# Kernel optimization log

Hardware: AMD Instinct MI355X
Metric: run time of the kernel (lower is better)

The kernel has to match this reference:

```python
import jax, jax.numpy as jnp
import numpy as np
from jax import lax

ANCHOR_AREAS = (128.0**2, 256.0**2, 512.0**2)
ASPECT_RATIOS = (0.5, 1.0, 2.0)
STRIDE = 32.0                      # resnet backbone: get_orig_stat maps fm -> input via x*32
PRE_NMS_TOP_N = 2000
POST_NMS_TOP_N = 100
NMS_IOU_T = 0.7
SCORE_T = 0.1
MIN_SCALE = 0.01
BBOX_XFORM_CLIP = float(np.log(1000.0 / 16.0))


def make_anchors(H, W):
    # anchors laid out in (H, W, A) order to match the offset permutation below
    sizes = []
    for area in ANCHOR_AREAS:
        for r in ASPECT_RATIOS:          # aspect_ratio = w / h
            sizes.append((np.sqrt(area * r), np.sqrt(area / r)))
    sizes = jnp.asarray(np.asarray(sizes, dtype=np.float32))  # [A, 2] (w, h)
    cy = (jnp.arange(H, dtype=jnp.float32) + 0.5) * STRIDE
    cx = (jnp.arange(W, dtype=jnp.float32) + 0.5) * STRIDE
    cyg, cxg = jnp.meshgrid(cy, cx, indexing='ij')             # [H, W]
    cxg = cxg[:, :, None]
    cyg = cyg[:, :, None]
    w = sizes[:, 0]
    h = sizes[:, 1]
    anchors = jnp.stack([cxg - w / 2, cyg - h / 2, cxg + w / 2, cyg + h / 2], axis=-1)
    return anchors.reshape(-1, 4)                              # [H*W*A, 4] xyxy


def decode_boxes(anchors, offsets):
    # anchors [N,4], offsets [B,N,4] (tx, ty, tw, th) -> boxes [B,N,4] xyxy
    wa = anchors[:, 2] - anchors[:, 0]
    ha = anchors[:, 3] - anchors[:, 1]
    cxa = anchors[:, 0] + 0.5 * wa
    cya = anchors[:, 1] + 0.5 * ha
    tx, ty = offsets[..., 0], offsets[..., 1]
    tw = jnp.minimum(offsets[..., 2], BBOX_XFORM_CLIP)
    th = jnp.minimum(offsets[..., 3], BBOX_XFORM_CLIP)
    px = tx * wa + cxa
    py = ty * ha + cya
    pw = jnp.exp(tw) * wa
    ph = jnp.exp(th) * ha
    return jnp.stack([px - pw / 2, py - ph / 2, px + pw / 2, py + ph / 2], axis=-1)


def box_iou(a, b):
    area_a = (a[:, 2] - a[:, 0]) * (a[:, 3] - a[:, 1])
    area_b = (b[:, 2] - b[:, 0]) * (b[:, 3] - b[:, 1])
    lt = jnp.maximum(a[:, None, :2], b[None, :, :2])
    rb = jnp.minimum(a[:, None, 2:], b[None, :, 2:])
    wh = jnp.clip(rb - lt, 0.0)
    inter = wh[..., 0] * wh[..., 1]
    return inter / (area_a[:, None] + area_b[None, :] - inter + 1e-9)


def nms_single(boxes, scores):
    # boxes [P,4] sorted by descending score; invalid entries carry score -1
    P = boxes.shape[0]
    iou = box_iou(boxes, boxes)
    idx = jnp.arange(P)

    def body(i, keep):
        sup = (iou[i] > NMS_IOU_T) & (idx > i)
        return jnp.where(keep[i], keep & (~sup), keep)

    keep = lax.stop_gradient(lax.fori_loop(0, P, body, scores > 0.0))
    kept_scores = jnp.where(keep, scores, -1.0)
    top_s, top_i = lax.top_k(kept_scores, POST_NMS_TOP_N)
    return boxes[top_i], top_s


def rpn_forward(features, W1, b1, W2, b2, W3, b3):
    B, Cin, H, W = features.shape
    A = W3.shape[0]
    # 3x3 sliding conv + ReLU
    t = lax.conv_general_dilated(
        features, W1, window_strides=(1, 1), padding='SAME',
        dimension_numbers=('NCHW', 'OIHW', 'NCHW'))
    t = jax.nn.relu(t + b1[None, :, None, None])
    # 1x1 sibling heads as channel contractions
    offs = jnp.einsum('bchw,oc->bohw', t, W2) + b2[None, :, None, None]   # [B, A*4, H, W]
    logits = jnp.einsum('bchw,oc->bohw', t, W3) + b3[None, :, None, None]  # [B, A, H, W]
    # reorder to per-anchor layout (H, W, A)
    offs = offs.reshape(B, A, 4, H, W).transpose(0, 3, 4, 1, 2).reshape(B, -1, 4)
    scores = jax.nn.sigmoid(logits.transpose(0, 2, 3, 1).reshape(B, -1))  # [B, N]
    anchors = make_anchors(H, W)
    boxes = decode_boxes(anchors, offs)                                    # [B, N, 4]
    # clip to image boundary (handle_cross_boundary_boxes during testing)
    img_w, img_h = W * STRIDE, H * STRIDE
    boxes = jnp.stack([
        jnp.clip(boxes[..., 0], 0.0, img_w),
        jnp.clip(boxes[..., 1], 0.0, img_h),
        jnp.clip(boxes[..., 2], 0.0, img_w),
        jnp.clip(boxes[..., 3], 0.0, img_h)], axis=-1)
    # score-threshold + min-scale filtering
    bw = boxes[..., 2] - boxes[..., 0]
    bh = boxes[..., 3] - boxes[..., 1]
    valid = (scores >= SCORE_T) & (bw > MIN_SCALE * img_w) & (bh > MIN_SCALE * img_h)
    masked = jnp.where(valid, scores, -1.0)
    # pre-NMS top-k, then per-image NMS + post-NMS top-n
    top_s, top_i = lax.top_k(masked, PRE_NMS_TOP_N)                        # [B, P]
    top_boxes = jnp.take_along_axis(boxes, top_i[..., None], axis=1)       # [B, P, 4]
    out_boxes, out_scores = jax.vmap(nms_single)(top_boxes, top_s)
    return out_boxes, out_scores                                           # [B,100,4], [B,100]


def setup_inputs() -> dict:
    key = jax.random.key(0)
    ks = jax.random.split(key, 4)
    B, Cin, H, W = 8, 1024, 50, 50
    A = 9
    C = 512
    return {
        'features': jax.random.normal(ks[0], (B, Cin, H, W), jnp.float32),
        'W1': jax.random.normal(ks[1], (C, Cin, 3, 3), jnp.float32) * 0.01,
        'b1': jnp.zeros((C,), jnp.float32),
        'W2': jax.random.normal(ks[2], (A * 4, C), jnp.float32) * 0.01,
        'b2': jnp.zeros((A * 4,), jnp.float32),
        'W3': jax.random.normal(ks[3], (A, C), jnp.float32) * 0.01,
        'b3': jnp.zeros((A,), jnp.float32),
    }


def reference(features, W1, b1, W2, b2, W3, b3):
    return rpn_forward(features, W1, b1, W2, b2, W3, b3)
```

## Files before the change

kernel.cpp:

```cpp
#include <hip/hip_runtime.h>
#include <cstdint>

#define NB 8
#define CIN 1024
#define HDIM 50
#define WDIM 50
#define COUT 512
#define NA 9
#define NANCH (HDIM*WDIM*NA)
#define PRE_N 2000
#define POST_N 100

typedef __attribute__((ext_vector_type(8))) short bf16x8;
typedef __attribute__((ext_vector_type(4))) float f32x4;
typedef __attribute__((ext_vector_type(16))) float f32x16;
typedef __attribute__((ext_vector_type(8))) unsigned short ushort8v;

constexpr size_t TPLANE    = 20578304;
constexpr size_t OFF_TPH   = 0;
constexpr size_t OFF_TPL   = OFF_TPH + TPLANE;
constexpr size_t OFF_BOXES = 41156608;
constexpr size_t OFF_MS    = OFF_BOXES + 2880000;
constexpr size_t OFF_KEYS  = OFF_MS + 720000;
constexpr size_t OFF_TBOX  = OFF_KEYS + 1440000;
constexpr size_t OFF_TS    = OFF_TBOX + 256000;
constexpr size_t OFF_SUP   = OFF_TS + 64000;
constexpr size_t OFF_KEEP  = OFF_SUP + 4096000;
constexpr size_t PPLANE    = 44318720;
constexpr size_t OFF_PH    = 50614656;
constexpr size_t OFF_PL    = OFF_PH + PPLANE;
constexpr size_t WPLANE    = 9437184;
constexpr size_t OFF_WH    = OFF_PL + PPLANE;
constexpr size_t OFF_WL    = OFF_WH + WPLANE;

__device__ __forceinline__ void split2bf16(float v, unsigned short &hi, unsigned short &lo) {
    unsigned int u = __float_as_uint(v);
    unsigned int r = u + 0x7FFFu + ((u >> 16) & 1u);
    hi = (unsigned short)(r >> 16);
    float hf = __uint_as_float(((unsigned int)hi) << 16);
    float lf = v - hf;
    unsigned int u2 = __float_as_uint(lf);
    unsigned int r2 = u2 + 0x7FFFu + ((u2 >> 16) & 1u);
    lo = (unsigned short)(r2 >> 16);
}

__device__ __forceinline__ void gl_lds(const unsigned short* g, unsigned short* l) {
    __builtin_amdgcn_global_load_lds(
        (const __attribute__((address_space(1))) unsigned int*)(const void*)g,
        (__attribute__((address_space(3))) unsigned int*)(void*)l,
        16, 0, 0);
}

__global__ __launch_bounds__(256) void prep_feat(const float* __restrict__ f,
                                                 unsigned short* __restrict__ Ph,
                                                 unsigned short* __restrict__ Pl) {
    int id = blockIdx.x * 256 + threadIdx.x;
    int cc = id % 52; int r = id / 52;
    int rr = r % 52;  r /= 52;
    int cic = r % 64; int b = r / 64;
    int h = rr - 1, w = cc - 1;
    bool inb = (h >= 0 && h < HDIM && w >= 0 && w < WDIM);
    ushort8v hv0, lv0, hv1, lv1;
#pragma unroll
    for (int j = 0; j < 16; ++j) {
        float v = 0.f;
        if (inb) v = f[(((size_t)b * CIN + cic * 16 + j) * HDIM + h) * WDIM + w];
        unsigned short hi, lo;
        split2bf16(v, hi, lo);
        if (j < 8) { hv0[j] = hi; lv0[j] = lo; }
        else       { hv1[j - 8] = hi; lv1[j - 8] = lo; }
    }
    size_t rowb = (size_t)((b * 64 + cic) * 52 + rr) * 832;
    *(ushort8v*)&Ph[rowb + cc * 8]       = hv0;
    *(ushort8v*)&Ph[rowb + 416 + cc * 8] = hv1;
    *(ushort8v*)&Pl[rowb + cc * 8]       = lv0;
    *(ushort8v*)&Pl[rowb + 416 + cc * 8] = lv1;
}

__global__ __launch_bounds__(256) void prep_w(const float* __restrict__ W1,
                                              unsigned short* __restrict__ Wh,
                                              unsigned short* __restrict__ Wl) {
    int id = blockIdx.x * 256 + threadIdx.x;
    int co = id % 32; int r = id / 32;
    int cic = r % 64; int cot = r / 64;
    int cog = cot * 32 + co;
    const float* src = W1 + ((size_t)cog * CIN + cic * 16) * 9;
    float v[144];
#pragma unroll
    for (int i = 0; i < 36; ++i) {
        float4 x = ((const float4*)src)[i];
        v[i * 4 + 0] = x.x; v[i * 4 + 1] = x.y; v[i * 4 + 2] = x.z; v[i * 4 + 3] = x.w;
    }
#pragma unroll
    for (int tap = 0; tap < 9; ++tap) {
        ushort8v hv0, lv0, hv1, lv1;
#pragma unroll
        for (int j = 0; j < 16; ++j) {
            unsigned short hi, lo;
            split2bf16(v[j * 9 + tap], hi, lo);
            if (j < 8) { hv0[j] = hi; lv0[j] = lo; }
            else       { hv1[j - 8] = hi; lv1[j - 8] = lo; }
        }
        size_t base = ((((size_t)(cot * 64 + cic)) * 9 + tap) * 2) * 256;
        *(ushort8v*)&Wh[base + co * 8]       = hv0;
        *(ushort8v*)&Wh[base + 256 + co * 8] = hv1;
        *(ushort8v*)&Wl[base + co * 8]       = lv0;
        *(ushort8v*)&Wl[base + 256 + co * 8] = lv1;
    }
}

__global__ __launch_bounds__(256, 4) void conv_mfma(const unsigned short* __restrict__ FPh,
                                                    const unsigned short* __restrict__ FPl,
                                                    const unsigned short* __restrict__ WPh,
                                                    const unsigned short* __restrict__ WPl,
                                                    const float* __restrict__ b1,
                                                    unsigned short* __restrict__ Tph,
                                                    unsigned short* __restrict__ Tpl) {
    __shared__ unsigned short sAh[5120], sAl[5120];
    __shared__ unsigned short sBh[4608], sBl[4608];

    int blk = blockIdx.x;
    int cot = blk & 15;
    int mt  = (blk >> 4) % 13;
    int b   = blk / 208;
    int co0 = cot * 32;
    int r0  = mt * 4;

    int t = threadIdx.x, wv = t >> 6, ln = t & 63;
    int lm = ln & 31, lk = ln >> 5;

    f32x16 acc[2];
#pragma unroll
    for (int jm = 0; jm < 2; ++jm)
#pragma unroll
        for (int rg = 0; rg < 16; ++rg) acc[jm][rg] = 0.f;

#pragma unroll 1
    for (int cic = 0; cic < 64; ++cic) {
        __syncthreads();
        const unsigned short* wH = WPh + (size_t)(cot * 64 + cic) * 4608;
        const unsigned short* wL = WPl + (size_t)(cot * 64 + cic) * 4608;
        const unsigned short* aH = FPh + (size_t)((b * 64 + cic) * 52 + r0) * 832;
        const unsigned short* aL = FPl + (size_t)((b * 64 + cic) * 52 + r0) * 832;
        if (wv == 0) {
#pragma unroll
            for (int s = 0; s < 9; ++s) gl_lds(wH + s * 512 + ln * 8, &sBh[s * 512]);
        } else if (wv == 1) {
#pragma unroll
            for (int s = 0; s < 9; ++s) gl_lds(wL + s * 512 + ln * 8, &sBl[s * 512]);
        } else if (wv == 2) {
#pragma unroll
            for (int s = 0; s < 10; ++s) gl_lds(aH + s * 512 + ln * 8, &sAh[s * 512]);
        } else {
#pragma unroll
            for (int s = 0; s < 10; ++s) gl_lds(aL + s * 512 + ln * 8, &sAl[s * 512]);
        }
        __syncthreads();

#pragma unroll
        for (int tap = 0; tap < 9; ++tap) {
            const int kh = tap / 3, kw = tap % 3;
            int arow = wv + kh;
            bf16x8 a[2][2], bh, bl;
#pragma unroll
            for (int jm = 0; jm < 2; ++jm) {
                int cc = jm * 32 + lm + kw;
                if (cc > 51) cc = 51;
                int ad = ((arow * 2 + lk) * 52 + cc) * 8;
                a[jm][0] = *(const bf16x8*)&sAh[ad];
                a[jm][1] = *(const bf16x8*)&sAl[ad];
            }
            {
                int bd = ((tap * 2 + lk) * 32 + lm) * 8;
                bh = *(const bf16x8*)&sBh[bd];
                bl = *(const bf16x8*)&sBl[bd];
            }
#pragma unroll
            for (int jm = 0; jm < 2; ++jm) {
                acc[jm] = __builtin_amdgcn_mfma_f32_32x32x16_bf16(a[jm][0], bh, acc[jm], 0, 0, 0);
                acc[jm] = __builtin_amdgcn_mfma_f32_32x32x16_bf16(a[jm][0], bl, acc[jm], 0, 0, 0);
                acc[jm] = __builtin_amdgcn_mfma_f32_32x32x16_bf16(a[jm][1], bh, acc[jm], 0, 0, 0);
            }
        }
    }

    int h = r0 + wv;
    if (h >= HDIM) return;
    int co = co0 + lm;
    float bv = b1[co];
#pragma unroll
    for (int jm = 0; jm < 2; ++jm) {
#pragma unroll
        for (int rg = 0; rg < 16; ++rg) {
            int w = jm * 32 + (rg & 3) + 8 * (rg >> 2) + 4 * lk;
            if (w < WDIM) {
                float v = fmaxf(acc[jm][rg] + bv, 0.f);
                unsigned short hi, lo;
                split2bf16(v, hi, lo);
                int px = b * 2500 + h * 50 + w;
                size_t sa = (((((size_t)(px >> 7) * 16 + (co >> 5)) * 8 + ((px >> 4) & 7)) * 4
                              + ((co >> 3) & 3)) * 16 + (px & 15)) * 8 + (co & 7);
                Tph[sa] = hi;
                Tpl[sa] = lo;
            }
        }
    }
}

__global__ __launch_bounds__(256) void proj_decode_mfma(const unsigned short* __restrict__ Tph,
                                                        const unsigned short* __restrict__ Tpl,
                                                        const float* __restrict__ W2,
                                                        const float* __restrict__ b2,
                                                        const float* __restrict__ W3,
                                                        const float* __restrict__ b3,
                                                        float* __restrict__ boxes,
                                                        unsigned long long* __restrict__ keys) {
    __shared__ unsigned short sTh[4096], sTl[4096];
    __shared__ unsigned short sWh[1536], sWl[1536];
    __shared__ float pout[128 * 46];

    int blk = blockIdx.x;
    int px0 = blk * 128;
    int t = threadIdx.x, wv = t >> 6, ln = t & 63;
    int lm = ln & 15, q = ln >> 4;

    f32x4 acc[2][3];
#pragma unroll
    for (int jm = 0; jm < 2; ++jm)
#pragma unroll
        for (int nf = 0; nf < 3; ++nf) acc[jm][nf] = (f32x4){0.f, 0.f, 0.f, 0.f};

#pragma unroll 1
    for (int cc16 = 0; cc16 < 16; ++cc16) {
        __syncthreads();
        size_t base = ((size_t)blk * 16 + cc16) * 4096;
        if (wv == 0) {
#pragma unroll
            for (int s = 0; s < 4; ++s) gl_lds(Tph + base + s * 512 + ln * 8, &sTh[s * 512]);
        } else if (wv == 1) {
#pragma unroll
            for (int s = 4; s < 8; ++s) gl_lds(Tph + base + s * 512 + ln * 8, &sTh[s * 512]);
        } else if (wv == 2) {
#pragma unroll
            for (int s = 0; s < 4; ++s) gl_lds(Tpl + base + s * 512 + ln * 8, &sTl[s * 512]);
        } else {
#pragma unroll
            for (int s = 4; s < 8; ++s) gl_lds(Tpl + base + s * 512 + ln * 8, &sTl[s * 512]);
        }
        int c0 = cc16 * 32;
        for (int idx = t; idx < 1536; idx += 256) {
            int o = idx >> 5, ci = idx & 31;
            float v = 0.f;
            if (o < 36) v = W2[o * 512 + c0 + ci];
            else if (o < 45) v = W3[(o - 36) * 512 + c0 + ci];
            unsigned short hi, lo;
            split2bf16(v, hi, lo);
            int ad = (((o >> 4) * 4 + (ci >> 3)) * 16 + (o & 15)) * 8 + (ci & 7);
            sWh[ad] = hi; sWl[ad] = lo;
        }
        __syncthreads();

        bf16x8 a[2][2], bb[3][2];
#pragma unroll
        for (int jm = 0; jm < 2; ++jm) {
            int mf = wv * 2 + jm;
            int ad = ((mf * 4 + q) * 16 + lm) * 8;
            a[jm][0] = *(const bf16x8*)&sTh[ad];
            a[jm][1] = *(const bf16x8*)&sTl[ad];
        }
#pragma unroll
        for (int nf = 0; nf < 3; ++nf) {
            int ad = ((nf * 4 + q) * 16 + lm) * 8;
            bb[nf][0] = *(const bf16x8*)&sWh[ad];
            bb[nf][1] = *(const bf16x8*)&sWl[ad];
        }
#pragma unroll
        for (int jm = 0; jm < 2; ++jm)
#pragma unroll
            for (int nf = 0; nf < 3; ++nf) {
                acc[jm][nf] = __builtin_amdgcn_mfma_f32_16x16x32_bf16(a[jm][0], bb[nf][0], acc[jm][nf], 0, 0, 0);
                acc[jm][nf] = __builtin_amdgcn_mfma_f32_16x16x32_bf16(a[jm][0], bb[nf][1], acc[jm][nf], 0, 0, 0);
                acc[jm][nf] = __builtin_amdgcn_mfma_f32_16x16x32_bf16(a[jm][1], bb[nf][0], acc[jm][nf], 0, 0, 0);
            }
    }
    __syncthreads();
#pragma unroll
    for (int jm = 0; jm < 2; ++jm)
#pragma unroll
        for (int nf = 0; nf < 3; ++nf) {
            int o = nf * 16 + lm;
            if (o < 45) {
                float bias = (o < 36) ? b2[o] : b3[o - 36];
#pragma unroll
                for (int rg = 0; rg < 4; ++rg) {
                    int pxl = (wv * 2 + jm) * 16 + q * 4 + rg;
                    pout[pxl * 46 + o] = acc[jm][nf][rg] + bias;
                }
            }
        }
    __syncthreads();

    const float AW[9] = {90.50966799187809f, 128.0f, 181.01933598375618f,
                         181.01933598375618f, 256.0f, 362.03867196751236f,
                         362.03867196751236f, 512.0f, 724.0773439350247f};
    const float AH[9] = {181.01933598375618f, 128.0f, 90.50966799187809f,
                         362.03867196751236f, 256.0f, 181.01933598375618f,
                         724.0773439350247f, 512.0f, 362.03867196751236f};
    const float CLIPV = 4.135166556742356f;
    const float IMG = 1600.0f;

    for (int it = t; it < 128 * 9; it += 256) {
        int pxl = it / 9, a = it - pxl * 9;
        int pxg = px0 + pxl;
        if (pxg >= 20000) continue;
        int b = pxg / 2500, rem = pxg % 2500;
        int h = rem / 50, w = rem % 50;

        float tx = pout[pxl * 46 + a * 4 + 0];
        float ty = pout[pxl * 46 + a * 4 + 1];
        float tw = pout[pxl * 46 + a * 4 + 2];
        float th = pout[pxl * 46 + a * 4 + 3];
        float lg = pout[pxl * 46 + 36 + a];

        float s = 1.0f / (1.0f + expf(-lg));

        float cx = ((float)w + 0.5f) * 32.0f;
        float cy = ((float)h + 0.5f) * 32.0f;
        float x1a = cx - 0.5f * AW[a];
        float x2a = cx + 0.5f * AW[a];
        float y1a = cy - 0.5f * AH[a];
        float y2a = cy + 0.5f * AH[a];
        float waf = x2a - x1a;
        float haf = y2a - y1a;
        float cxa = x1a + 0.5f * waf;
        float cya = y1a + 0.5f * haf;

        float twc = tw < CLIPV ? tw : CLIPV;
        float thc = th < CLIPV ? th : CLIPV;
        float pxc = tx * waf + cxa;
        float pyc = ty * haf + cya;
        float pw  = expf(twc) * waf;
        float ph  = expf(thc) * haf;

        float x1 = pxc - 0.5f * pw;
        float y1 = pyc - 0.5f * ph;
        float x2 = pxc + 0.5f * pw;
        float y2 = pyc + 0.5f * ph;
        x1 = fminf(fmaxf(x1, 0.f), IMG);
        y1 = fminf(fmaxf(y1, 0.f), IMG);
        x2 = fminf(fmaxf(x2, 0.f), IMG);
        y2 = fminf(fmaxf(y2, 0.f), IMG);

        float bw = x2 - x1, bh = y2 - y1;
        bool valid = (s >= 0.1f) && (bw > 16.0f) && (bh > 16.0f);
        float m = valid ? s : -1.0f;

        int idx = (h * WDIM + w) * NA + a;
        size_t gi = (size_t)b * NANCH + idx;
        ((float4*)boxes)[gi] = make_float4(x1, y1, x2, y2);
        unsigned int u = __float_as_uint(m);
        unsigned int k32 = (u & 0x80000000u) ? ~u : (u | 0x80000000u);
        keys[gi] = ((unsigned long long)k32 << 15) | (unsigned long long)(32767 - idx);
    }
}

__global__ __launch_bounds__(1024) void select_sort_kernel(const unsigned long long* __restrict__ keys,
                                                           const float* __restrict__ boxes,
                                                           float* __restrict__ top_boxes,
                                                           float* __restrict__ top_s) {
    int b = blockIdx.x;
    int t = threadIdx.x;
    int wv = t >> 6;
    const unsigned long long* kb = keys + (size_t)b * NANCH;

    __shared__ unsigned int whist[16][256];
    __shared__ unsigned int hist[256];
    __shared__ int s_chosen, s_rnew;
    __shared__ unsigned int s_cnt;
    __shared__ unsigned long long skeys[2048];

    const int widths[6] = {8, 8, 8, 8, 8, 7};
    unsigned long long prefix = 0;
    int bitsdone = 0;
    int r = PRE_N;

    for (int p = 0; p < 6; ++p) {
        int width = widths[p];
        int bins = 1 << width;
        int shift = 47 - bitsdone - width;
        for (int i = t; i < 16 * 256; i += 1024) ((unsigned int*)whist)[i] = 0;
        __syncthreads();
        for (int i = t; i < NANCH; i += 1024) {
            unsigned long long k = kb[i];
            if ((k >> (47 - bitsdone)) == prefix)
                atomicAdd(&whist[wv][(unsigned)((k >> shift) & (unsigned long long)(bins - 1))], 1u);
        }
        __syncthreads();
        if (t < bins) {
            unsigned int s = 0;
#pragma unroll
            for (int w = 0; w < 16; ++w) s += whist[w][t];
            hist[t] = s;
        }
        __syncthreads();
        if (t == 0) {
            int acc = 0, chosen = 0, rnew = 1;
            for (int d = bins - 1; d >= 0; --d) {
                int hv = (int)hist[d];
                if (acc + hv >= r) { chosen = d; rnew = r - acc; break; }
                acc += hv;
            }
            s_chosen = chosen;
            s_rnew = rnew;
        }
        __syncthreads();
        prefix = (prefix << width) | (unsigned long long)s_chosen;
        bitsdone += width;
        r = s_rnew;
        __syncthreads();
    }
    unsigned long long Kst = prefix;

    if (t == 0) s_cnt = 0;
    __syncthreads();
    for (int i = t; i < NANCH; i += 1024) {
        unsigned long long k = kb[i];
        if (k >= Kst) {
            unsigned int p = atomicAdd(&s_cnt, 1u);
            if (p < 2048) skeys[p] = k;
        }
    }
    __syncthreads();
    unsigned int cnt = s_cnt;
    for (int i = t; i < 2048; i += 1024)
        if (i >= (int)cnt) skeys[i] = 0ull;
    for (int k = 2; k <= 2048; k <<= 1) {
        for (int j = k >> 1; j > 0; j >>= 1) {
            __syncthreads();
            for (int i = t; i < 2048; i += 1024) {
                int l = i ^ j;
                if (l > i) {
                    unsigned long long a = skeys[i], c = skeys[l];
                    bool up = ((i & k) == 0);
                    if (up ? (a < c) : (a > c)) { skeys[i] = c; skeys[l] = a; }
                }
            }
        }
    }
    __syncthreads();
    for (int i = t; i < PRE_N; i += 1024) {
        unsigned long long k = skeys[i];
        unsigned int k32 = (unsigned int)(k >> 15);
        float m = (k32 & 0x80000000u) ? __uint_as_float(k32 & 0x7FFFFFFFu)
                                      : __uint_as_float(~k32);
        unsigned int idx = 32767u - (unsigned int)(k & 32767ull);
        size_t gi = (size_t)b * NANCH + idx;
        top_s[b * PRE_N + i] = m;
        ((float4*)top_boxes)[b * PRE_N + i] = ((const float4*)boxes)[gi];
    }
}

__global__ __launch_bounds__(256) void sup_kernel(const float* __restrict__ top_boxes,
                                                  unsigned long long* __restrict__ supm) {
    int blk = blockIdx.x;
    int b = blk / 125;
    int chunk = blk % 125;
    int t = threadIdx.x;

    __shared__ float bx1[PRE_N], by1[PRE_N], bx2[PRE_N], by2[PRE_N];
    for (int i = t; i < PRE_N; i += 256) {
        float4 v = ((const float4*)top_boxes)[b * PRE_N + i];
        bx1[i] = v.x; by1[i] = v.y; bx2[i] = v.z; by2[i] = v.w;
    }
    __syncthreads();

    int wave = t >> 6, lane = t & 63;
    for (int rr = 0; rr < 4; ++rr) {
        int i = chunk * 16 + wave * 4 + rr;
        float ax1 = bx1[i], ay1 = by1[i], ax2 = bx2[i], ay2 = by2[i];
        float aarea = (ax2 - ax1) * (ay2 - ay1);
        for (int jw = 0; jw < 32; ++jw) {
            int j = jw * 64 + lane;
            bool sup = false;
            if (j > i && j < PRE_N) {
                float jx1 = bx1[j], jy1 = by1[j], jx2 = bx2[j], jy2 = by2[j];
                float ix1 = fmaxf(ax1, jx1), iy1 = fmaxf(ay1, jy1);
                float ix2 = fminf(ax2, jx2), iy2 = fminf(ay2, jy2);
                float iw = fmaxf(ix2 - ix1, 0.f);
                float ih = fmaxf(iy2 - iy1, 0.f);
                float inter = iw * ih;
                float barea = (jx2 - jx1) * (jy2 - jy1);
                float iou = inter / (aarea + barea - inter + 1e-9f);
                sup = iou > 0.7f;
            }
            unsigned long long m = __ballot(sup);
            if (lane == 0) supm[((size_t)b * PRE_N + i) * 32 + jw] = m;
        }
    }
}

__global__ __launch_bounds__(256) void nms_fin_kernel(const float* __restrict__ top_s,
                                                      const unsigned long long* __restrict__ supm,
                                                      const float* __restrict__ top_boxes,
                                                      float* __restrict__ out) {
    int b = blockIdx.x;
    int t = threadIdx.x;
    __shared__ unsigned int kw[64];
    __shared__ int wpre[65];

    if (t < 64) {
        int lane = t;
        unsigned int alive = 0;
        for (int q = 0; q < 32; ++q) {
            int i = lane * 32 + q;
            if (i < PRE_N && top_s[b * PRE_N + i] > 0.f) alive |= (1u << q);
        }
        const unsigned long long* sm = supm + (size_t)b * PRE_N * 32;
        const unsigned int* sup32 = (const unsigned int*)sm;

        for (int tt = 0; tt < 32; ++tt) {
            unsigned int alo = __shfl(alive, 2 * tt);
            unsigned int ahi = __shfl(alive, 2 * tt + 1);
            unsigned long long talive = (unsigned long long)alo | ((unsigned long long)ahi << 32);
            int i_row = tt * 64 + lane;
            unsigned long long rm = (i_row < PRE_N) ? sm[(size_t)i_row * 32 + tt] : 0ull;

            unsigned long long kept = 0, rem = talive;
            while (rem) {
                int j = __builtin_ctzll(rem);
                kept |= (1ull << j);
                unsigned long long rmj = __shfl(rm, j);
                rem &= ~rmj;
                rem &= ~(1ull << j);
            }

            unsigned int oracc = 0;
            unsigned long long kk = kept;
            while (kk) {
                int j0 = __builtin_ctzll(kk); kk &= kk - 1;
                int j1 = -1, j2 = -1, j3 = -1;
                if (kk) { j1 = __builtin_ctzll(kk); kk &= kk - 1; }
                if (kk) { j2 = __builtin_ctzll(kk); kk &= kk - 1; }
                if (kk) { j3 = __builtin_ctzll(kk); kk &= kk - 1; }
                unsigned int v0 = sup32[(size_t)(tt * 64 + j0) * 64 + lane];
                unsigned int v1 = (j1 >= 0) ? sup32[(size_t)(tt * 64 + j1) * 64 + lane] : 0u;
                unsigned int v2 = (j2 >= 0) ? sup32[(size_t)(tt * 64 + j2) * 64 + lane] : 0u;
                unsigned int v3 = (j3 >= 0) ? sup32[(size_t)(tt * 64 + j3) * 64 + lane] : 0u;
                oracc |= v0 | v1 | v2 | v3;
            }
            alive &= ~oracc;
            if (lane == 2 * tt)     alive = (unsigned int)kept;
            if (lane == 2 * tt + 1) alive = (unsigned int)(kept >> 32);
        }
        kw[lane] = alive;
    }
    __syncthreads();
    if (t == 0) {
        int run = 0;
        for (int w = 0; w < 64; ++w) { wpre[w] = run; run += __popc(kw[w]); }
        wpre[64] = run;
    }
    __syncthreads();
    int total = wpre[64];
    float* out_boxes  = out;
    float* out_scores = out + NB * POST_N * 4;
    for (int i = t; i < PRE_N; i += 256) {
        unsigned int w = kw[i >> 5];
        bool kept = (w >> (i & 31)) & 1u;
        int rk = wpre[i >> 5] + __popc(w & ((1u << (i & 31)) - 1u));
        int pos = kept ? rk : total + (i - rk);
        if (pos < POST_N) {
            out_scores[b * POST_N + pos] = kept ? top_s[b * PRE_N + i] : -1.0f;
            ((float4*)out_boxes)[b * POST_N + pos] = ((const float4*)top_boxes)[b * PRE_N + i];
        }
    }
}

extern "C" void kernel_launch(void* const* d_in, const int* in_sizes, int n_in,
                              void* d_out, int out_size, void* d_ws, size_t ws_size,
                              hipStream_t stream) {
    const float* features = (const float*)d_in[0];
    const float* W1 = (const float*)d_in[1];
    const float* b1 = (const float*)d_in[2];
    const float* W2 = (const float*)d_in[3];
    const float* b2 = (const float*)d_in[4];
    const float* W3 = (const float*)d_in[5];
    const float* b3 = (const float*)d_in[6];
    float* out = (float*)d_out;
    char* ws = (char*)d_ws;

    unsigned short* Tph = (unsigned short*)(ws + OFF_TPH);
    unsigned short* Tpl = (unsigned short*)(ws + OFF_TPL);
    float* boxes   = (float*)(ws + OFF_BOXES);
    unsigned long long* keys = (unsigned long long*)(ws + OFF_KEYS);
    float* top_boxes = (float*)(ws + OFF_TBOX);
    float* top_s     = (float*)(ws + OFF_TS);
    unsigned long long* supm = (unsigned long long*)(ws + OFF_SUP);
    unsigned short* FPh = (unsigned short*)(ws + OFF_PH);
    unsigned short* FPl = (unsigned short*)(ws + OFF_PL);
    unsigned short* WPh = (unsigned short*)(ws + OFF_WH);
    unsigned short* WPl = (unsigned short*)(ws + OFF_WL);

    prep_feat<<<5408, 256, 0, stream>>>(features, FPh, FPl);
    prep_w<<<128, 256, 0, stream>>>(W1, WPh, WPl);
    conv_mfma<<<1664, 256, 0, stream>>>(FPh, FPl, WPh, WPl, b1, Tph, Tpl);
    proj_decode_mfma<<<157, 256, 0, stream>>>(Tph, Tpl, W2, b2, W3, b3, boxes, keys);
    select_sort_kernel<<<NB, 1024, 0, stream>>>(keys, boxes, top_boxes, top_s);
    sup_kernel<<<NB * 125, 256, 0, stream>>>(top_boxes, supm);
    nms_fin_kernel<<<NB, 256, 0, stream>>>(top_s, supm, top_boxes, out);
}
```

Measured before the change: 1.152 ms.

## Flatten padded feature plane and enlarge conv tile to 256 pixels by 64 channels

The padded feature map is stored as a flat 1D plane per channel chunk with a halo margin, so the 3x3 conv is computed as shifted 1D windows over 256-pixel tiles. Each block now covers 64 output channels instead of 32, and each wave holds a 2x2 grid of MFMA accumulators. The aim is more reuse of every LDS load per MFMA and fewer blocks reloading the same data. The two prep kernels are merged into one launch. The cost is a larger LDS footprint, occupancy capped at 2 blocks per CU, and some wasted compute on padding columns.

```diff
diff --git a/kernel.cpp b/kernel.cpp
--- a/kernel.cpp
+++ b/kernel.cpp
@@ -18,19 +18,19 @@
 
 constexpr size_t TPLANE    = 20578304;
 constexpr size_t OFF_TPH   = 0;
-constexpr size_t OFF_TPL   = OFF_TPH + TPLANE;
+constexpr size_t OFF_TPL   = 20578304;
 constexpr size_t OFF_BOXES = 41156608;
-constexpr size_t OFF_MS    = OFF_BOXES + 2880000;
-constexpr size_t OFF_KEYS  = OFF_MS + 720000;
-constexpr size_t OFF_TBOX  = OFF_KEYS + 1440000;
-constexpr size_t OFF_TS    = OFF_TBOX + 256000;
-constexpr size_t OFF_SUP   = OFF_TS + 64000;
-constexpr size_t OFF_KEEP  = OFF_SUP + 4096000;
-constexpr size_t PPLANE    = 44318720;
-constexpr size_t OFF_PH    = 50614656;
+constexpr size_t OFF_KEYS  = 44036608;
+constexpr size_t OFF_TBOX  = 45476608;
+constexpr size_t OFF_TS    = 45732608;
+constexpr size_t OFF_SUP   = 45796608;
+constexpr size_t QDIM      = 2976;
+constexpr size_t PLSTRIDE  = QDIM * 8;
+constexpr size_t PPLANE    = 48758784;
+constexpr size_t OFF_PH    = 49892864;
 constexpr size_t OFF_PL    = OFF_PH + PPLANE;
 constexpr size_t WPLANE    = 9437184;
-constexpr size_t OFF_WH    = OFF_PL + PPLANE;
+constexpr size_t OFF_WH    = 147410432;
 constexpr size_t OFF_WL    = OFF_WH + WPLANE;
 
 __device__ __forceinline__ void split2bf16(float v, unsigned short &hi, unsigned short &lo) {
@@ -51,157 +51,170 @@
         16, 0, 0);
 }
 
-__global__ __launch_bounds__(256) void prep_feat(const float* __restrict__ f,
-                                                 unsigned short* __restrict__ Ph,
-                                                 unsigned short* __restrict__ Pl) {
-    int id = blockIdx.x * 256 + threadIdx.x;
-    int cc = id % 52; int r = id / 52;
-    int rr = r % 52;  r /= 52;
-    int cic = r % 64; int b = r / 64;
-    int h = rr - 1, w = cc - 1;
-    bool inb = (h >= 0 && h < HDIM && w >= 0 && w < WDIM);
-    ushort8v hv0, lv0, hv1, lv1;
-#pragma unroll
-    for (int j = 0; j < 16; ++j) {
-        float v = 0.f;
-        if (inb) v = f[(((size_t)b * CIN + cic * 16 + j) * HDIM + h) * WDIM + w];
-        unsigned short hi, lo;
-        split2bf16(v, hi, lo);
-        if (j < 8) { hv0[j] = hi; lv0[j] = lo; }
-        else       { hv1[j - 8] = hi; lv1[j - 8] = lo; }
-    }
-    size_t rowb = (size_t)((b * 64 + cic) * 52 + rr) * 832;
-    *(ushort8v*)&Ph[rowb + cc * 8]       = hv0;
-    *(ushort8v*)&Ph[rowb + 416 + cc * 8] = hv1;
-    *(ushort8v*)&Pl[rowb + cc * 8]       = lv0;
-    *(ushort8v*)&Pl[rowb + 416 + cc * 8] = lv1;
-}
-
-__global__ __launch_bounds__(256) void prep_w(const float* __restrict__ W1,
-                                              unsigned short* __restrict__ Wh,
-                                              unsigned short* __restrict__ Wl) {
-    int id = blockIdx.x * 256 + threadIdx.x;
-    int co = id % 32; int r = id / 32;
-    int cic = r % 64; int cot = r / 64;
-    int cog = cot * 32 + co;
-    const float* src = W1 + ((size_t)cog * CIN + cic * 16) * 9;
-    float v[144];
-#pragma unroll
-    for (int i = 0; i < 36; ++i) {
-        float4 x = ((const float4*)src)[i];
-        v[i * 4 + 0] = x.x; v[i * 4 + 1] = x.y; v[i * 4 + 2] = x.z; v[i * 4 + 3] = x.w;
-    }
-#pragma unroll
-    for (int tap = 0; tap < 9; ++tap) {
+__global__ __launch_bounds__(256) void prep_all(const float* __restrict__ f,
+                                                const float* __restrict__ W1,
+                                                unsigned short* __restrict__ Ph,
+                                                unsigned short* __restrict__ Pl,
+                                                unsigned short* __restrict__ Wh,
+                                                unsigned short* __restrict__ Wl) {
+    int blk = blockIdx.x;
+    if (blk < 5952) {
+        int id = blk * 256 + threadIdx.x;
+        int q = id % (int)QDIM; int r = id / (int)QDIM;
+        int cic = r % 64; int b = r / 64;
+        int pp = q - 53;
+        int rr = pp / 52, cc = pp - rr * 52;
+        int h = rr - 1, w = cc - 1;
+        bool inb = (pp >= 0) && (pp < 2704) && (h >= 0) && (h < HDIM) && (w >= 0) && (w < WDIM);
         ushort8v hv0, lv0, hv1, lv1;
 #pragma unroll
         for (int j = 0; j < 16; ++j) {
+            float v = 0.f;
+            if (inb) v = f[(((size_t)b * CIN + cic * 16 + j) * HDIM + h) * WDIM + w];
             unsigned short hi, lo;
-            split2bf16(v[j * 9 + tap], hi, lo);
+            split2bf16(v, hi, lo);
             if (j < 8) { hv0[j] = hi; lv0[j] = lo; }
             else       { hv1[j - 8] = hi; lv1[j - 8] = lo; }
         }
-        size_t base = ((((size_t)(cot * 64 + cic)) * 9 + tap) * 2) * 256;
-        *(ushort8v*)&Wh[base + co * 8]       = hv0;
-        *(ushort8v*)&Wh[base + 256 + co * 8] = hv1;
-        *(ushort8v*)&Wl[base + co * 8]       = lv0;
-        *(ushort8v*)&Wl[base + 256 + co * 8] = lv1;
-    }
-}
-
-__global__ __launch_bounds__(256, 4) void conv_mfma(const unsigned short* __restrict__ FPh,
+        size_t b0 = ((size_t)((b * 64 + cic) * 2 + 0)) * PLSTRIDE + (size_t)q * 8;
+        size_t b1 = ((size_t)((b * 64 + cic) * 2 + 1)) * PLSTRIDE + (size_t)q * 8;
+        *(ushort8v*)&Ph[b0] = hv0;
+        *(ushort8v*)&Ph[b1] = hv1;
+        *(ushort8v*)&Pl[b0] = lv0;
+        *(ushort8v*)&Pl[b1] = lv1;
+    } else {
+        int id = (blk - 5952) * 256 + threadIdx.x;
+        int co = id % 64; int r = id / 64;
+        int cic = r % 64; int cot = r / 64;
+        int cog = cot * 64 + co;
+        const float* src = W1 + ((size_t)cog * CIN + cic * 16) * 9;
+        float v[144];
+#pragma unroll
+        for (int i = 0; i < 36; ++i) {
+            float4 x = ((const float4*)src)[i];
+            v[i * 4 + 0] = x.x; v[i * 4 + 1] = x.y; v[i * 4 + 2] = x.z; v[i * 4 + 3] = x.w;
+        }
+#pragma unroll
+        for (int tap = 0; tap < 9; ++tap) {
+            ushort8v hv0, lv0, hv1, lv1;
+#pragma unroll
+            for (int j = 0; j < 16; ++j) {
+                unsigned short hi, lo;
+                split2bf16(v[j * 9 + tap], hi, lo);
+                if (j < 8) { hv0[j] = hi; lv0[j] = lo; }
+                else       { hv1[j - 8] = hi; lv1[j - 8] = lo; }
+            }
+            size_t base = (((size_t)(cot * 64 + cic) * 9 + tap) * 2) * 512;
+            *(ushort8v*)&Wh[base + co * 8]       = hv0;
+            *(ushort8v*)&Wh[base + 512 + co * 8] = hv1;
+            *(ushort8v*)&Wl[base + co * 8]       = lv0;
+            *(ushort8v*)&Wl[base + 512 + co * 8] = lv1;
+        }
+    }
+}
+
+__global__ __launch_bounds__(256, 2) void conv_mfma(const unsigned short* __restrict__ FPh,
                                                     const unsigned short* __restrict__ FPl,
                                                     const unsigned short* __restrict__ WPh,
                                                     const unsigned short* __restrict__ WPl,
                                                     const float* __restrict__ b1,
                                                     unsigned short* __restrict__ Tph,
                                                     unsigned short* __restrict__ Tpl) {
-    __shared__ unsigned short sAh[5120], sAl[5120];
-    __shared__ unsigned short sBh[4608], sBl[4608];
+    __shared__ unsigned short sA[2][2][3072];
+    __shared__ unsigned short sB[2][9216];
 
     int blk = blockIdx.x;
-    int cot = blk & 15;
-    int mt  = (blk >> 4) % 13;
-    int b   = blk / 208;
-    int co0 = cot * 32;
-    int r0  = mt * 4;
+    int cot = blk & 7;
+    int ptile = (blk >> 3) % 11;
+    int b = blk / 88;
+    int co0 = cot * 64;
+    int P0 = 32 + ptile * 256;
 
     int t = threadIdx.x, wv = t >> 6, ln = t & 63;
     int lm = ln & 31, lk = ln >> 5;
 
-    f32x16 acc[2];
+    f32x16 acc[2][2];
 #pragma unroll
     for (int jm = 0; jm < 2; ++jm)
 #pragma unroll
-        for (int rg = 0; rg < 16; ++rg) acc[jm][rg] = 0.f;
+        for (int jn = 0; jn < 2; ++jn)
+#pragma unroll
+            for (int rg = 0; rg < 16; ++rg) acc[jm][jn][rg] = 0.f;
 
 #pragma unroll 1
     for (int cic = 0; cic < 64; ++cic) {
         __syncthreads();
-        const unsigned short* wH = WPh + (size_t)(cot * 64 + cic) * 4608;
-        const unsigned short* wL = WPl + (size_t)(cot * 64 + cic) * 4608;
-        const unsigned short* aH = FPh + (size_t)((b * 64 + cic) * 52 + r0) * 832;
-        const unsigned short* aL = FPl + (size_t)((b * 64 + cic) * 52 + r0) * 832;
-        if (wv == 0) {
-#pragma unroll
-            for (int s = 0; s < 9; ++s) gl_lds(wH + s * 512 + ln * 8, &sBh[s * 512]);
-        } else if (wv == 1) {
-#pragma unroll
-            for (int s = 0; s < 9; ++s) gl_lds(wL + s * 512 + ln * 8, &sBl[s * 512]);
-        } else if (wv == 2) {
-#pragma unroll
-            for (int s = 0; s < 10; ++s) gl_lds(aH + s * 512 + ln * 8, &sAh[s * 512]);
-        } else {
-#pragma unroll
-            for (int s = 0; s < 10; ++s) gl_lds(aL + s * 512 + ln * 8, &sAl[s * 512]);
+#pragma unroll
+        for (int k = 0; k < 15; ++k) {
+            int id = wv * 15 + k;
+            if (id < 24) {
+                int hl = id / 12, lkc = (id / 6) & 1, s = id % 6;
+                const unsigned short* pl = hl ? FPl : FPh;
+                const unsigned short* src = pl
+                    + ((size_t)((b * 64 + cic) * 2 + lkc)) * PLSTRIDE
+                    + (size_t)P0 * 8 + s * 512 + ln * 8;
+                gl_lds(src, &sA[hl][lkc][s * 512]);
+            } else {
+                int j = id - 24;
+                int hl = j / 18, s = j % 18;
+                const unsigned short* pl = hl ? WPl : WPh;
+                const unsigned short* src = pl + (size_t)(cot * 64 + cic) * 9216 + s * 512 + ln * 8;
+                gl_lds(src, &sB[hl][s * 512]);
+            }
         }
         __syncthreads();
 
 #pragma unroll
         for (int tap = 0; tap < 9; ++tap) {
             const int kh = tap / 3, kw = tap % 3;
-            int arow = wv + kh;
-            bf16x8 a[2][2], bh, bl;
+            const int dlt = (kh - 1) * 52 + (kw - 1);
+            bf16x8 a[2][2], bb[2][2];
 #pragma unroll
             for (int jm = 0; jm < 2; ++jm) {
-                int cc = jm * 32 + lm + kw;
-                if (cc > 51) cc = 51;
-                int ad = ((arow * 2 + lk) * 52 + cc) * 8;
-                a[jm][0] = *(const bf16x8*)&sAh[ad];
-                a[jm][1] = *(const bf16x8*)&sAl[ad];
-            }
-            {
-                int bd = ((tap * 2 + lk) * 32 + lm) * 8;
-                bh = *(const bf16x8*)&sBh[bd];
-                bl = *(const bf16x8*)&sBl[bd];
-            }
-#pragma unroll
-            for (int jm = 0; jm < 2; ++jm) {
-                acc[jm] = __builtin_amdgcn_mfma_f32_32x32x16_bf16(a[jm][0], bh, acc[jm], 0, 0, 0);
-                acc[jm] = __builtin_amdgcn_mfma_f32_32x32x16_bf16(a[jm][0], bl, acc[jm], 0, 0, 0);
-                acc[jm] = __builtin_amdgcn_mfma_f32_32x32x16_bf16(a[jm][1], bh, acc[jm], 0, 0, 0);
-            }
-        }
-    }
-
-    int h = r0 + wv;
-    if (h >= HDIM) return;
-    int co = co0 + lm;
-    float bv = b1[co];
-#pragma unroll
-    for (int jm = 0; jm < 2; ++jm) {
-#pragma unroll
-        for (int rg = 0; rg < 16; ++rg) {
-            int w = jm * 32 + (rg & 3) + 8 * (rg >> 2) + 4 * lk;
-            if (w < WDIM) {
-                float v = fmaxf(acc[jm][rg] + bv, 0.f);
-                unsigned short hi, lo;
-                split2bf16(v, hi, lo);
-                int px = b * 2500 + h * 50 + w;
-                size_t sa = (((((size_t)(px >> 7) * 16 + (co >> 5)) * 8 + ((px >> 4) & 7)) * 4
-                              + ((co >> 3) & 3)) * 16 + (px & 15)) * 8 + (co & 7);
-                Tph[sa] = hi;
-                Tpl[sa] = lo;
+                int e = (wv * 2 + jm) * 32 + lm + dlt + 53;
+                int ad = e * 8;
+                a[jm][0] = *(const bf16x8*)&sA[0][lk][ad];
+                a[jm][1] = *(const bf16x8*)&sA[1][lk][ad];
+            }
+#pragma unroll
+            for (int jn = 0; jn < 2; ++jn) {
+                int bd = tap * 1024 + lk * 512 + (jn * 32 + lm) * 8;
+                bb[jn][0] = *(const bf16x8*)&sB[0][bd];
+                bb[jn][1] = *(const bf16x8*)&sB[1][bd];
+            }
+#pragma unroll
+            for (int jm = 0; jm < 2; ++jm)
+#pragma unroll
+                for (int jn = 0; jn < 2; ++jn) {
+                    acc[jm][jn] = __builtin_amdgcn_mfma_f32_32x32x16_bf16(a[jm][0], bb[jn][0], acc[jm][jn], 0, 0, 0);
+                    acc[jm][jn] = __builtin_amdgcn_mfma_f32_32x32x16_bf16(a[jm][0], bb[jn][1], acc[jm][jn], 0, 0, 0);
+                    acc[jm][jn] = __builtin_amdgcn_mfma_f32_32x32x16_bf16(a[jm][1], bb[jn][0], acc[jm][jn], 0, 0, 0);
+                }
+        }
+    }
+
+#pragma unroll
+    for (int jn = 0; jn < 2; ++jn) {
+        int co = co0 + jn * 32 + lm;
+        float bv = b1[co];
+#pragma unroll
+        for (int jm = 0; jm < 2; ++jm) {
+#pragma unroll
+            for (int rg = 0; rg < 16; ++rg) {
+                int mrow = (rg & 3) + 8 * (rg >> 2) + 4 * lk;
+                int pp = P0 + (wv * 2 + jm) * 32 + mrow;
+                int rr = pp / 52, cc = pp - rr * 52;
+                int h = rr - 1, w = cc - 1;
+                if ((unsigned)h < HDIM && (unsigned)w < WDIM) {
+                    float v = fmaxf(acc[jm][jn][rg] + bv, 0.f);
+                    unsigned short hi, lo;
+                    split2bf16(v, hi, lo);
+                    int px = b * 2500 + h * 50 + w;
+                    size_t sa = (((((size_t)(px >> 7) * 16 + (co >> 5)) * 8 + ((px >> 4) & 7)) * 4
+                                  + ((co >> 3) & 3)) * 16 + (px & 15)) * 8 + (co & 7);
+                    Tph[sa] = hi;
+                    Tpl[sa] = lo;
+                }
             }
         }
     }
@@ -601,9 +614,8 @@
     unsigned short* WPh = (unsigned short*)(ws + OFF_WH);
     unsigned short* WPl = (unsigned short*)(ws + OFF_WL);
 
-    prep_feat<<<5408, 256, 0, stream>>>(features, FPh, FPl);
-    prep_w<<<128, 256, 0, stream>>>(W1, WPh, WPl);
-    conv_mfma<<<1664, 256, 0, stream>>>(FPh, FPl, WPh, WPl, b1, Tph, Tpl);
+    prep_all<<<6080, 256, 0, stream>>>(features, W1, FPh, FPl, WPh, WPl);
+    conv_mfma<<<704, 256, 0, stream>>>(FPh, FPl, WPh, WPl, b1, Tph, Tpl);
     proj_decode_mfma<<<157, 256, 0, stream>>>(Tph, Tpl, W2, b2, W3, b3, boxes, keys);
     select_sort_kernel<<<NB, 1024, 0, stream>>>(keys, boxes, top_boxes, top_s);
     sup_kernel<<<NB * 125, 256, 0, stream>>>(top_boxes, supm);
```

Result: faster. 1.117 ms (-3.0%).
